# Performance work log

Measured on AMD Instinct MI355X. Metric: run time of the kernel, lower is better.

## Reference

```python
import jax, jax.numpy as jnp
import numpy as np

N_NODES = 50000
N_EDGES = 800000
D = 128


def _graph_conv(x, W, b, src, dst, n_nodes):
    """DGL GraphConv with norm='both': D_in^{-1/2} A D_out^{-1/2} X W + b."""
    ones = jnp.ones((src.shape[0],), dtype=x.dtype)
    out_deg = jax.ops.segment_sum(ones, src, num_segments=n_nodes)
    in_deg = jax.ops.segment_sum(ones, dst, num_segments=n_nodes)
    out_norm = jax.lax.rsqrt(jnp.maximum(out_deg, 1.0))  # [N]
    in_norm = jax.lax.rsqrt(jnp.maximum(in_deg, 1.0))    # [N]
    # scale src features, transform (in_feats == out_feats so order is free), aggregate
    h = (x * out_norm[:, None]) @ W                       # [N, D]
    msgs = h[src]                                         # [E, D] gather
    agg = jax.ops.segment_sum(msgs, dst, num_segments=n_nodes)  # [N, D] scatter-add
    return agg * in_norm[:, None] + b


def setup_inputs() -> dict:
    key = jax.random.key(0)
    ks = jax.random.split(key, 8)
    x = jax.random.normal(ks[0], (N_NODES, D), dtype=jnp.float32)
    src = jax.random.randint(ks[1], (N_EDGES,), 0, N_NODES, dtype=jnp.int64)
    dst = jax.random.randint(ks[2], (N_EDGES,), 0, N_NODES, dtype=jnp.int64)
    scale = 1.0 / np.sqrt(D)
    W1 = jax.random.normal(ks[3], (D, D), dtype=jnp.float32) * scale
    W2 = jax.random.normal(ks[4], (D, D), dtype=jnp.float32) * scale
    W3 = jax.random.normal(ks[5], (D, D), dtype=jnp.float32) * scale
    b1 = jnp.zeros((D,), dtype=jnp.float32)
    b2 = jnp.zeros((D,), dtype=jnp.float32)
    b3 = jnp.zeros((D,), dtype=jnp.float32)
    return {"x": x, "src": src, "dst": dst,
            "W1": W1, "b1": b1, "W2": W2, "b2": b2, "W3": W3, "b3": b3}


def reference(x, src, dst, W1, b1, W2, b2, W3, b3):
    h = _graph_conv(x, W1, b1, src, dst, N_NODES)
    h = jax.nn.relu(h)
    h = _graph_conv(h, W2, b2, src, dst, N_NODES)
    h = jax.nn.relu(h)
    h = _graph_conv(h, W3, b3, src, dst, N_NODES)
    return h
```

## Files before the change

### kernel.cpp

```cpp
#include <hip/hip_runtime.h>
#include <hip/hip_fp16.h>

#define D 128
#define HB 128
#define HT 1024
#define WMAX 12800

struct alignas(16) H8 { __half2 h[4]; };
typedef _Float16 v8h __attribute__((ext_vector_type(8)));
typedef float v4f __attribute__((ext_vector_type(4)));

__global__ __launch_bounds__(HT) void hist_kernel(const int* __restrict__ src,
                                                  const int* __restrict__ dst,
                                                  unsigned* __restrict__ partial_out,
                                                  unsigned* __restrict__ partial_in,
                                                  unsigned char* __restrict__ lrank,
                                                  const float* __restrict__ W1,
                                                  const float* __restrict__ W2,
                                                  const float* __restrict__ W3,
                                                  _Float16* __restrict__ wt,
                                                  int nE, int W, int epb) {
    const int t = threadIdx.x;
    if ((int)blockIdx.x >= 2 * HB) {
        const int l = blockIdx.x - 2 * HB;
        const float* Wsrc = (l == 0) ? W1 : ((l == 1) ? W2 : W3);
        _Float16* o = wt + (size_t)l * D * D;
        for (int i = t; i < D * D; i += HT) {
            const int k = i >> 7, n = i & 127;
            o[n * D + k] = (_Float16)Wsrc[i];
        }
        return;
    }
    __shared__ unsigned lcnt[WMAX];
    const bool is_dst = (blockIdx.x < HB);
    const int b = is_dst ? blockIdx.x : (blockIdx.x - HB);
    for (int i = t; i < W; i += HT) lcnt[i] = 0;
    __syncthreads();
    const int e0 = b * epb;
    const int e1 = min(nE, e0 + epb);
    if (is_dst) {
        for (int e = e0 + t; e < e1; e += HT) {
            const int d = dst[e];
            const unsigned sh = (unsigned)(d & 3) * 8u;
            const unsigned old = atomicAdd(&lcnt[d >> 2], 1u << sh);
            lrank[e] = (unsigned char)((old >> sh) & 0xffu);
        }
    } else {
        for (int e = e0 + t; e < e1; e += HT) {
            const int s = src[e];
            atomicAdd(&lcnt[s >> 2], 1u << ((unsigned)(s & 3) * 8u));
        }
    }
    __syncthreads();
    unsigned* g = (is_dst ? partial_in : partial_out) + (size_t)b * W;
    for (int i = t; i < W; i += HT) g[i] = lcnt[i];
}

__global__ __launch_bounds__(256) void reduce_hist_kernel(const unsigned* __restrict__ partial_out,
                                                          const unsigned* __restrict__ partial_in,
                                                          unsigned* __restrict__ offs_in,
                                                          int* __restrict__ cnt_out,
                                                          int* __restrict__ cnt_in,
                                                          int W, int n, int nbW) {
    const bool is_dst = ((int)blockIdx.x < nbW);
    const int w = (is_dst ? blockIdx.x : (blockIdx.x - nbW)) * 256 + threadIdx.x;
    if (w >= W) return;
    unsigned run = 0;
    if (is_dst) {
#pragma unroll 16
        for (int b = 0; b < HB; ++b) {
            const unsigned c = partial_in[(size_t)b * W + w];
            offs_in[(size_t)b * W + w] = run;
            run += c;
        }
    } else {
#pragma unroll 16
        for (int b = 0; b < HB; ++b) run += partial_out[(size_t)b * W + w];
    }
    int* cnt = is_dst ? cnt_in : cnt_out;
    const int n0 = w * 4;
    const int4 c4 = make_int4((int)(run & 0xffu), (int)((run >> 8) & 0xffu),
                              (int)((run >> 16) & 0xffu), (int)((run >> 24) & 0xffu));
    if (n0 + 3 < n) {
        *(int4*)&cnt[n0] = c4;
    } else {
        const int* cp = &c4.x;
        for (int i = 0; i < 4 && n0 + i < n; ++i) cnt[n0 + i] = cp[i];
    }
}

__global__ __launch_bounds__(1024) void scan_block_kernel(const int* __restrict__ deg,
                                                          int* __restrict__ rp,
                                                          int* __restrict__ bsum, int n) {
    __shared__ int wsum[16];
    const int t = threadIdx.x;
    const int lane = t & 63;
    const int wid = t >> 6;
    const int i = blockIdx.x * 1024 + t;
    const int v = (i < n) ? deg[i] : 0;
    int s = v;
#pragma unroll
    for (int off = 1; off < 64; off <<= 1) {
        int u = __shfl_up(s, off, 64);
        if (lane >= off) s += u;
    }
    if (lane == 63) wsum[wid] = s;
    __syncthreads();
    if (wid == 0) {
        int ws = (lane < 16) ? wsum[lane] : 0;
#pragma unroll
        for (int off = 1; off < 16; off <<= 1) {
            int u = __shfl_up(ws, off, 64);
            if (lane >= off) ws += u;
        }
        if (lane < 16) wsum[lane] = ws;
    }
    __syncthreads();
    const int excl = s - v + ((wid > 0) ? wsum[wid - 1] : 0);
    if (i < n) rp[i] = excl;
    if (t == 0) bsum[blockIdx.x] = wsum[15];
}

__global__ __launch_bounds__(1024) void finalize_kernel(int* __restrict__ rp,
                                                        const int* __restrict__ bsum,
                                                        const int* __restrict__ cnt_out,
                                                        const int* __restrict__ cnt_in,
                                                        float* __restrict__ onorm,
                                                        float* __restrict__ inorm,
                                                        int n, int nb, int nE) {
    __shared__ int prefix_s;
    const int t = threadIdx.x;
    if (t < 64) {
        int v = (t < nb && t < (int)blockIdx.x) ? bsum[t] : 0;
#pragma unroll
        for (int off = 1; off < 64; off <<= 1) v += __shfl_xor(v, off, 64);
        if (t == 0) prefix_s = v;
    }
    __syncthreads();
    const int i = blockIdx.x * 1024 + t;
    if (i < n) {
        rp[i] += prefix_s;
        onorm[i] = rsqrtf(fmaxf((float)cnt_out[i], 1.0f));
        inorm[i] = rsqrtf(fmaxf((float)cnt_in[i], 1.0f));
    }
    if (blockIdx.x == 0 && t == 0) rp[n] = nE;
}

__global__ __launch_bounds__(1024) void gemm1_fill_kernel(
    const float* __restrict__ x, const _Float16* __restrict__ wt,
    const float* __restrict__ onorm, __half* __restrict__ y1, int nrows,
    const int* __restrict__ src, const int* __restrict__ dst,
    const unsigned char* __restrict__ lrank, const unsigned* __restrict__ offs_in,
    const int* __restrict__ rp, int* __restrict__ srcs_sorted,
    int nE, int epb, int W, int nGemmBlocks) {
    __shared__ _Float16 sA[128 * 136];
    __shared__ _Float16 sB[128 * 136];
    const int t = threadIdx.x;

    if ((int)blockIdx.x >= nGemmBlocks) {
        const int e = (blockIdx.x - nGemmBlocks) * 1024 + t;
        if (e < nE) {
            const int d = dst[e];
            const int b = e / epb;
            const unsigned off =
                (offs_in[(size_t)b * W + (d >> 2)] >> ((unsigned)(d & 3) * 8u)) & 0xffu;
            srcs_sorted[rp[d] + (int)off + (int)lrank[e]] = src[e];
        }
        return;
    }

    const int row0 = blockIdx.x * 128;
    const int rr = t >> 4;
    const int c8 = t & 15;
#pragma unroll
    for (int pass = 0; pass < 2; ++pass) {
        const int row = pass * 64 + rr;
        *(float4*)&sB[row * 136 + c8 * 8] = *(const float4*)&wt[(size_t)row * D + c8 * 8];
        const int grow = row0 + row;
        float4 u0 = make_float4(0.f, 0.f, 0.f, 0.f);
        float4 u1 = u0;
        if (grow < nrows) {
            const float* ap = x + (size_t)grow * D + c8 * 8;
            u0 = ((const float4*)ap)[0];
            u1 = ((const float4*)ap)[1];
        }
        v8h hv;
        hv[0] = (_Float16)u0.x; hv[1] = (_Float16)u0.y;
        hv[2] = (_Float16)u0.z; hv[3] = (_Float16)u0.w;
        hv[4] = (_Float16)u1.x; hv[5] = (_Float16)u1.y;
        hv[6] = (_Float16)u1.z; hv[7] = (_Float16)u1.w;
        *(v8h*)&sA[row * 136 + c8 * 8] = hv;
    }
    __syncthreads();

    const int w = t >> 6;
    const int lane = t & 63;
    const int m16 = lane & 15;
    const int quad = lane >> 4;
    const int rt = w >> 1;
    const int ch = w & 1;

    v4f c[4];
#pragma unroll
    for (int ct = 0; ct < 4; ++ct) c[ct] = (v4f){0.f, 0.f, 0.f, 0.f};

#pragma unroll
    for (int ks = 0; ks < 4; ++ks) {
        const v8h a = *(const v8h*)&sA[(rt * 16 + m16) * 136 + ks * 32 + quad * 8];
#pragma unroll
        for (int ct = 0; ct < 4; ++ct) {
            const v8h b = *(const v8h*)&sB[((ch * 4 + ct) * 16 + m16) * 136 + ks * 32 + quad * 8];
            c[ct] = __builtin_amdgcn_mfma_f32_16x16x32_f16(a, b, c[ct], 0, 0, 0);
        }
    }

#pragma unroll
    for (int r = 0; r < 4; ++r) {
        const int row = row0 + rt * 16 + quad * 4 + r;
        if (row < nrows) {
            const float osc = onorm[row];
#pragma unroll
            for (int ct = 0; ct < 4; ++ct) {
                const int col = (ch * 4 + ct) * 16 + m16;
                y1[(size_t)row * D + col] = __float2half(c[ct][r] * osc);
            }
        }
    }
}

template <bool EPI>
__global__ __launch_bounds__(256) void aggregate_kernel(const __half* __restrict__ xh,
                                                        const float* __restrict__ onorm,
                                                        const float* __restrict__ inorm,
                                                        const float* __restrict__ bias,
                                                        const int* __restrict__ rp,
                                                        const int* __restrict__ srcs,
                                                        __half* __restrict__ agg, int n_nodes) {
    const int node = blockIdx.x * 4 + (threadIdx.x >> 6);
    const int lane = threadIdx.x & 63;
    const int rg = lane >> 4;
    const int c8 = lane & 15;
    if (node >= n_nodes) return;
    const int e0 = rp[node];
    const int e1 = rp[node + 1];

    float acc0[8], acc1[8];
#pragma unroll
    for (int j = 0; j < 8; ++j) { acc0[j] = 0.f; acc1[j] = 0.f; }

    auto accum = [&](float* acc, const H8 v) {
#pragma unroll
        for (int j = 0; j < 4; ++j) {
            acc[2 * j]     += __low2float(v.h[j]);
            acc[2 * j + 1] += __high2float(v.h[j]);
        }
    };

    int e = e0;
    for (; e + 16 <= e1; e += 16) {
        const int s0 = srcs[e + rg];
        const int s1 = srcs[e + 4 + rg];
        const int s2 = srcs[e + 8 + rg];
        const int s3 = srcs[e + 12 + rg];
        const H8 v0 = ((const H8*)(xh + (size_t)s0 * D))[c8];
        const H8 v1 = ((const H8*)(xh + (size_t)s1 * D))[c8];
        const H8 v2 = ((const H8*)(xh + (size_t)s2 * D))[c8];
        const H8 v3 = ((const H8*)(xh + (size_t)s3 * D))[c8];
        accum(acc0, v0); accum(acc1, v1); accum(acc0, v2); accum(acc1, v3);
    }
    for (; e + 4 <= e1; e += 4) {
        const int s0 = srcs[e + rg];
        accum(acc0, ((const H8*)(xh + (size_t)s0 * D))[c8]);
    }
    if (e < e1 && rg < (e1 - e)) {
        const int s0 = srcs[e + rg];
        accum(acc1, ((const H8*)(xh + (size_t)s0 * D))[c8]);
    }

    float r[8];
#pragma unroll
    for (int j = 0; j < 8; ++j) r[j] = acc0[j] + acc1[j];
#pragma unroll
    for (int off = 16; off < 64; off <<= 1)
#pragma unroll
        for (int j = 0; j < 8; ++j) r[j] += __shfl_xor(r[j], off, 64);

    if (rg == 0) {
        if (EPI) {
            const float inm = inorm[node];
            const float onm = onorm[node];
            const float4 bv0 = ((const float4*)bias)[c8 * 2];
            const float4 bv1 = ((const float4*)bias)[c8 * 2 + 1];
            const float* bp0 = &bv0.x;
            const float* bp1 = &bv1.x;
#pragma unroll
            for (int j = 0; j < 4; ++j) {
                r[j]     = fmaxf(fmaf(r[j],     inm, bp0[j]), 0.f) * onm;
                r[j + 4] = fmaxf(fmaf(r[j + 4], inm, bp1[j]), 0.f) * onm;
            }
        }
        H8 h;
#pragma unroll
        for (int j = 0; j < 4; ++j) h.h[j] = __floats2half2_rn(r[2 * j], r[2 * j + 1]);
        ((H8*)(agg + (size_t)node * D))[c8] = h;
    }
}

template <bool FULL, bool RELU, bool OSCALE, bool OUT16>
__global__ __launch_bounds__(256) void gemm_mfma_kernel(const __half* __restrict__ Ah,
                                                        const _Float16* __restrict__ Wt,
                                                        const float* __restrict__ bias,
                                                        const float* __restrict__ inorm,
                                                        const float* __restrict__ onorm,
                                                        void* __restrict__ outv, int nrows) {
    __shared__ _Float16 sA[128 * 136];
    __shared__ _Float16 sB[128 * 136];
    const int t = threadIdx.x;
    const int row0 = blockIdx.x * 128;
    const int rr = t >> 4;
    const int c8 = t & 15;

#pragma unroll
    for (int pass = 0; pass < 8; ++pass) {
        const int row = pass * 16 + rr;
        *(float4*)&sB[row * 136 + c8 * 8] = *(const float4*)&Wt[(size_t)row * D + c8 * 8];
        const int grow = row0 + row;
        float4 v = make_float4(0.f, 0.f, 0.f, 0.f);
        if (grow < nrows)
            v = *(const float4*)((const _Float16*)Ah + (size_t)grow * D + c8 * 8);
        *(float4*)&sA[row * 136 + c8 * 8] = v;
    }
    __syncthreads();

    const int w = t >> 6;
    const int lane = t & 63;
    const int m16 = lane & 15;
    const int quad = lane >> 4;

    v4f c[2][8];
#pragma unroll
    for (int rt = 0; rt < 2; ++rt)
#pragma unroll
        for (int ct = 0; ct < 8; ++ct) c[rt][ct] = (v4f){0.f, 0.f, 0.f, 0.f};

#pragma unroll
    for (int ks = 0; ks < 4; ++ks) {
        v8h afr[2], bfr[8];
#pragma unroll
        for (int rt = 0; rt < 2; ++rt)
            afr[rt] = *(const v8h*)&sA[(w * 32 + rt * 16 + m16) * 136 + ks * 32 + quad * 8];
#pragma unroll
        for (int ct = 0; ct < 8; ++ct)
            bfr[ct] = *(const v8h*)&sB[(ct * 16 + m16) * 136 + ks * 32 + quad * 8];
#pragma unroll
        for (int rt = 0; rt < 2; ++rt)
#pragma unroll
            for (int ct = 0; ct < 8; ++ct)
                c[rt][ct] = __builtin_amdgcn_mfma_f32_16x16x32_f16(afr[rt], bfr[ct], c[rt][ct], 0, 0, 0);
    }

#pragma unroll
    for (int rt = 0; rt < 2; ++rt) {
#pragma unroll
        for (int r = 0; r < 4; ++r) {
            const int row = row0 + w * 32 + rt * 16 + quad * 4 + r;
            if (row < nrows) {
                const float inm = FULL ? inorm[row] : 1.0f;
                const float osc = OSCALE ? onorm[row] : 1.0f;
#pragma unroll
                for (int ct = 0; ct < 8; ++ct) {
                    const int col = ct * 16 + m16;
                    float v = c[rt][ct][r];
                    if (FULL) v = fmaf(v, inm, bias[col]);
                    if (RELU) v = fmaxf(v, 0.f);
                    if (OSCALE) v *= osc;
                    if (OUT16) ((__half*)outv)[(size_t)row * D + col] = __float2half(v);
                    else       ((float*)outv)[(size_t)row * D + col] = v;
                }
            }
        }
    }
}

extern "C" void kernel_launch(void* const* d_in, const int* in_sizes, int n_in,
                              void* d_out, int out_size, void* d_ws, size_t ws_size,
                              hipStream_t stream) {
    const float* x   = (const float*)d_in[0];
    const int*   src = (const int*)d_in[1];
    const int*   dst = (const int*)d_in[2];
    const float* W1  = (const float*)d_in[3];
    const float* b1  = (const float*)d_in[4];
    const float* W2  = (const float*)d_in[5];
    const float* b2  = (const float*)d_in[6];
    const float* W3  = (const float*)d_in[7];
    const float* b3  = (const float*)d_in[8];

    const int N = in_sizes[0] / D;
    const int E = in_sizes[1];

    char* p = (char*)d_ws;
    auto alloc = [&](size_t bytes) -> void* {
        void* r = (void*)p;
        p += (bytes + 255) & ~(size_t)255;
        return r;
    };
    int*           cnt_out = (int*)alloc((size_t)N * 4);
    int*           cnt_in  = (int*)alloc((size_t)N * 4);
    int*           rp      = (int*)alloc((size_t)(N + 1) * 4);
    int*           bsum    = (int*)alloc(1024 * 4);
    float*         onorm   = (float*)alloc((size_t)N * 4);
    float*         inorm   = (float*)alloc((size_t)N * 4);
    int*           srcs    = (int*)alloc((size_t)E * 4);
    unsigned char* lrank   = (unsigned char*)alloc((size_t)E);
    _Float16*      wt      = (_Float16*)alloc((size_t)3 * D * D * 2);
    __half*        hbuf0   = (__half*)alloc((size_t)N * D * 2);
    __half*        hbuf1   = (__half*)alloc((size_t)N * D * 2);
    char*          scratch = (char*)alloc((size_t)3 * HB * ((N + 3) / 4) * 4);

    const int W = (N + 3) / 4;
    const int epb = (E + HB - 1) / HB;
    unsigned* partial_in  = (unsigned*)scratch;
    unsigned* partial_out = partial_in + (size_t)HB * W;
    unsigned* offs_in     = partial_out + (size_t)HB * W;
    __half*   abuf        = (__half*)scratch;
    float*    outf        = (float*)d_out;

    const int nb = (N + 1023) / 1024;
    const int nbW = (W + 255) / 256;
    const int gemmGrid = (N + 127) / 128;
    const int fillGrid = (E + 1023) / 1024;
    const int aggGrid = (N + 3) / 4;

    hist_kernel<<<2 * HB + 3, HT, 0, stream>>>(src, dst, partial_out, partial_in, lrank,
                                               W1, W2, W3, wt, E, W, epb);
    reduce_hist_kernel<<<2 * nbW, 256, 0, stream>>>(partial_out, partial_in, offs_in,
                                                    cnt_out, cnt_in, W, N, nbW);
    scan_block_kernel<<<nb, 1024, 0, stream>>>(cnt_in, rp, bsum, N);
    finalize_kernel<<<nb, 1024, 0, stream>>>(rp, bsum, cnt_out, cnt_in, onorm, inorm, N, nb, E);

    gemm1_fill_kernel<<<gemmGrid + fillGrid, 1024, 0, stream>>>(
        x, wt, onorm, hbuf0, N,
        src, dst, lrank, offs_in, rp, srcs, E, epb, W, gemmGrid);

    aggregate_kernel<true><<<aggGrid, 256, 0, stream>>>(
        hbuf0, onorm, inorm, b1, rp, srcs, hbuf1, N);
    aggregate_kernel<false><<<aggGrid, 256, 0, stream>>>(
        hbuf1, onorm, inorm, b2, rp, srcs, abuf, N);
    gemm_mfma_kernel<true, true, true, true><<<gemmGrid, 256, 0, stream>>>(
        abuf, wt + (size_t)D * D, b2, inorm, onorm, hbuf0, N);
    aggregate_kernel<false><<<aggGrid, 256, 0, stream>>>(
        hbuf0, onorm, inorm, b3, rp, srcs, abuf, N);
    gemm_mfma_kernel<true, false, false, false><<<gemmGrid, 256, 0, stream>>>(
        abuf, wt + (size_t)2 * D * D, b3, inorm, onorm, outf, N);
}
```

Measured before the change: 245.1 us.

## Fuse neighbor aggregation into GEMM for layers two and three

```diff
diff --git a/kernel.cpp b/kernel.cpp
--- a/kernel.cpp
+++ b/kernel.cpp
@@ -228,7 +228,6 @@
     }
 }
 
-template <bool EPI>
 __global__ __launch_bounds__(256) void aggregate_kernel(const __half* __restrict__ xh,
                                                         const float* __restrict__ onorm,
                                                         const float* __restrict__ inorm,
@@ -286,18 +285,16 @@
         for (int j = 0; j < 8; ++j) r[j] += __shfl_xor(r[j], off, 64);
 
     if (rg == 0) {
-        if (EPI) {
-            const float inm = inorm[node];
-            const float onm = onorm[node];
-            const float4 bv0 = ((const float4*)bias)[c8 * 2];
-            const float4 bv1 = ((const float4*)bias)[c8 * 2 + 1];
-            const float* bp0 = &bv0.x;
-            const float* bp1 = &bv1.x;
-#pragma unroll
-            for (int j = 0; j < 4; ++j) {
-                r[j]     = fmaxf(fmaf(r[j],     inm, bp0[j]), 0.f) * onm;
-                r[j + 4] = fmaxf(fmaf(r[j + 4], inm, bp1[j]), 0.f) * onm;
-            }
+        const float inm = inorm[node];
+        const float onm = onorm[node];
+        const float4 bv0 = ((const float4*)bias)[c8 * 2];
+        const float4 bv1 = ((const float4*)bias)[c8 * 2 + 1];
+        const float* bp0 = &bv0.x;
+        const float* bp1 = &bv1.x;
+#pragma unroll
+        for (int j = 0; j < 4; ++j) {
+            r[j]     = fmaxf(fmaf(r[j],     inm, bp0[j]), 0.f) * onm;
+            r[j + 4] = fmaxf(fmaf(r[j + 4], inm, bp1[j]), 0.f) * onm;
         }
         H8 h;
 #pragma unroll
@@ -306,76 +303,121 @@
     }
 }
 
-template <bool FULL, bool RELU, bool OSCALE, bool OUT16>
-__global__ __launch_bounds__(256) void gemm_mfma_kernel(const __half* __restrict__ Ah,
-                                                        const _Float16* __restrict__ Wt,
-                                                        const float* __restrict__ bias,
-                                                        const float* __restrict__ inorm,
-                                                        const float* __restrict__ onorm,
-                                                        void* __restrict__ outv, int nrows) {
-    __shared__ _Float16 sA[128 * 136];
+template <bool LAST>
+__global__ __launch_bounds__(256) void agg_gemm_kernel(const __half* __restrict__ xh,
+                                                       const _Float16* __restrict__ Wt,
+                                                       const float* __restrict__ bias,
+                                                       const float* __restrict__ inorm,
+                                                       const float* __restrict__ onorm,
+                                                       const int* __restrict__ rp,
+                                                       const int* __restrict__ srcs,
+                                                       void* __restrict__ outv, int n_nodes) {
+    __shared__ _Float16 sA[64 * 136];
     __shared__ _Float16 sB[128 * 136];
     const int t = threadIdx.x;
-    const int row0 = blockIdx.x * 128;
-    const int rr = t >> 4;
-    const int c8 = t & 15;
-
-#pragma unroll
-    for (int pass = 0; pass < 8; ++pass) {
-        const int row = pass * 16 + rr;
-        *(float4*)&sB[row * 136 + c8 * 8] = *(const float4*)&Wt[(size_t)row * D + c8 * 8];
-        const int grow = row0 + row;
-        float4 v = make_float4(0.f, 0.f, 0.f, 0.f);
-        if (grow < nrows)
-            v = *(const float4*)((const _Float16*)Ah + (size_t)grow * D + c8 * 8);
-        *(float4*)&sA[row * 136 + c8 * 8] = v;
-    }
-    __syncthreads();
+    const int tile0 = blockIdx.x * 64;
+
+    {
+        const int rr = t >> 4;
+        const int cc = t & 15;
+#pragma unroll
+        for (int p = 0; p < 8; ++p) {
+            const int row = p * 16 + rr;
+            *(float4*)&sB[row * 136 + cc * 8] = *(const float4*)&Wt[(size_t)row * D + cc * 8];
+        }
+    }
 
     const int w = t >> 6;
     const int lane = t & 63;
+    const int rg = lane >> 4;
+    const int c8 = lane & 15;
+
+    for (int i = 0; i < 16; ++i) {
+        const int lrow = w * 16 + i;
+        const int node = tile0 + lrow;
+        float r[8];
+#pragma unroll
+        for (int j = 0; j < 8; ++j) r[j] = 0.f;
+        if (node < n_nodes) {
+            const int e0 = rp[node];
+            const int e1 = rp[node + 1];
+            float acc1[8];
+#pragma unroll
+            for (int j = 0; j < 8; ++j) acc1[j] = 0.f;
+            auto accum = [&](float* acc, const H8 v) {
+#pragma unroll
+                for (int j = 0; j < 4; ++j) {
+                    acc[2 * j]     += __low2float(v.h[j]);
+                    acc[2 * j + 1] += __high2float(v.h[j]);
+                }
+            };
+            int e = e0;
+            for (; e + 16 <= e1; e += 16) {
+                const int s0 = srcs[e + rg];
+                const int s1 = srcs[e + 4 + rg];
+                const int s2 = srcs[e + 8 + rg];
+                const int s3 = srcs[e + 12 + rg];
+                const H8 v0 = ((const H8*)(xh + (size_t)s0 * D))[c8];
+                const H8 v1 = ((const H8*)(xh + (size_t)s1 * D))[c8];
+                const H8 v2 = ((const H8*)(xh + (size_t)s2 * D))[c8];
+                const H8 v3 = ((const H8*)(xh + (size_t)s3 * D))[c8];
+                accum(r, v0); accum(acc1, v1); accum(r, v2); accum(acc1, v3);
+            }
+            for (; e + 4 <= e1; e += 4) {
+                const int s0 = srcs[e + rg];
+                accum(r, ((const H8*)(xh + (size_t)s0 * D))[c8]);
+            }
+            if (e < e1 && rg < (e1 - e)) {
+                const int s0 = srcs[e + rg];
+                accum(acc1, ((const H8*)(xh + (size_t)s0 * D))[c8]);
+            }
+#pragma unroll
+            for (int j = 0; j < 8; ++j) r[j] += acc1[j];
+#pragma unroll
+            for (int off = 16; off < 64; off <<= 1)
+#pragma unroll
+                for (int j = 0; j < 8; ++j) r[j] += __shfl_xor(r[j], off, 64);
+        }
+        if (rg == 0) {
+            H8 h;
+#pragma unroll
+            for (int j = 0; j < 4; ++j) h.h[j] = __floats2half2_rn(r[2 * j], r[2 * j + 1]);
+            *(H8*)&sA[lrow * 136 + c8 * 8] = h;
+        }
+    }
+    __syncthreads();
+
     const int m16 = lane & 15;
     const int quad = lane >> 4;
-
-    v4f c[2][8];
-#pragma unroll
-    for (int rt = 0; rt < 2; ++rt)
-#pragma unroll
-        for (int ct = 0; ct < 8; ++ct) c[rt][ct] = (v4f){0.f, 0.f, 0.f, 0.f};
+    v4f c[8];
+#pragma unroll
+    for (int ct = 0; ct < 8; ++ct) c[ct] = (v4f){0.f, 0.f, 0.f, 0.f};
 
 #pragma unroll
     for (int ks = 0; ks < 4; ++ks) {
-        v8h afr[2], bfr[8];
-#pragma unroll
-        for (int rt = 0; rt < 2; ++rt)
-            afr[rt] = *(const v8h*)&sA[(w * 32 + rt * 16 + m16) * 136 + ks * 32 + quad * 8];
-#pragma unroll
-        for (int ct = 0; ct < 8; ++ct)
-            bfr[ct] = *(const v8h*)&sB[(ct * 16 + m16) * 136 + ks * 32 + quad * 8];
-#pragma unroll
-        for (int rt = 0; rt < 2; ++rt)
-#pragma unroll
-            for (int ct = 0; ct < 8; ++ct)
-                c[rt][ct] = __builtin_amdgcn_mfma_f32_16x16x32_f16(afr[rt], bfr[ct], c[rt][ct], 0, 0, 0);
-    }
-
-#pragma unroll
-    for (int rt = 0; rt < 2; ++rt) {
-#pragma unroll
-        for (int r = 0; r < 4; ++r) {
-            const int row = row0 + w * 32 + rt * 16 + quad * 4 + r;
-            if (row < nrows) {
-                const float inm = FULL ? inorm[row] : 1.0f;
-                const float osc = OSCALE ? onorm[row] : 1.0f;
-#pragma unroll
-                for (int ct = 0; ct < 8; ++ct) {
-                    const int col = ct * 16 + m16;
-                    float v = c[rt][ct][r];
-                    if (FULL) v = fmaf(v, inm, bias[col]);
-                    if (RELU) v = fmaxf(v, 0.f);
-                    if (OSCALE) v *= osc;
-                    if (OUT16) ((__half*)outv)[(size_t)row * D + col] = __float2half(v);
-                    else       ((float*)outv)[(size_t)row * D + col] = v;
+        const v8h a = *(const v8h*)&sA[(w * 16 + m16) * 136 + ks * 32 + quad * 8];
+#pragma unroll
+        for (int ct = 0; ct < 8; ++ct) {
+            const v8h b = *(const v8h*)&sB[(ct * 16 + m16) * 136 + ks * 32 + quad * 8];
+            c[ct] = __builtin_amdgcn_mfma_f32_16x16x32_f16(a, b, c[ct], 0, 0, 0);
+        }
+    }
+
+#pragma unroll
+    for (int r = 0; r < 4; ++r) {
+        const int row = tile0 + w * 16 + quad * 4 + r;
+        if (row < n_nodes) {
+            const float inm = inorm[row];
+            const float osc = LAST ? 1.0f : onorm[row];
+#pragma unroll
+            for (int ct = 0; ct < 8; ++ct) {
+                const int col = ct * 16 + m16;
+                float v = fmaf(c[ct][r], inm, bias[col]);
+                if (!LAST) {
+                    v = fmaxf(v, 0.f) * osc;
+                    ((__half*)outv)[(size_t)row * D + col] = __float2half(v);
+                } else {
+                    ((float*)outv)[(size_t)row * D + col] = v;
                 }
             }
         }
@@ -422,7 +464,6 @@
     unsigned* partial_in  = (unsigned*)scratch;
     unsigned* partial_out = partial_in + (size_t)HB * W;
     unsigned* offs_in     = partial_out + (size_t)HB * W;
-    __half*   abuf        = (__half*)scratch;
     float*    outf        = (float*)d_out;
 
     const int nb = (N + 1023) / 1024;
@@ -430,6 +471,7 @@
     const int gemmGrid = (N + 127) / 128;
     const int fillGrid = (E + 1023) / 1024;
     const int aggGrid = (N + 3) / 4;
+    const int fuseGrid = (N + 63) / 64;
 
     hist_kernel<<<2 * HB + 3, HT, 0, stream>>>(src, dst, partial_out, partial_in, lrank,
                                                W1, W2, W3, wt, E, W, epb);
@@ -442,14 +484,10 @@
         x, wt, onorm, hbuf0, N,
         src, dst, lrank, offs_in, rp, srcs, E, epb, W, gemmGrid);
 
-    aggregate_kernel<true><<<aggGrid, 256, 0, stream>>>(
+    aggregate_kernel<<<aggGrid, 256, 0, stream>>>(
         hbuf0, onorm, inorm, b1, rp, srcs, hbuf1, N);
-    aggregate_kernel<false><<<aggGrid, 256, 0, stream>>>(
-        hbuf1, onorm, inorm, b2, rp, srcs, abuf, N);
-    gemm_mfma_kernel<true, true, true, true><<<gemmGrid, 256, 0, stream>>>(
-        abuf, wt + (size_t)D * D, b2, inorm, onorm, hbuf0, N);
-    aggregate_kernel<false><<<aggGrid, 256, 0, stream>>>(
-        hbuf0, onorm, inorm, b3, rp, srcs, abuf, N);
-    gemm_mfma_kernel<true, false, false, false><<<gemmGrid, 256, 0, stream>>>(
-        abuf, wt + (size_t)2 * D * D, b3, inorm, onorm, outf, N);
-}
+    agg_gemm_kernel<false><<<fuseGrid, 256, 0, stream>>>(
+        hbuf1, wt + (size_t)D * D, b2, inorm, onorm, rp, srcs, hbuf0, N);
+    agg_gemm_kernel<true><<<fuseGrid, 256, 0, stream>>>(
+        hbuf0, wt + (size_t)2 * D * D, b3, inorm, onorm, rp, srcs, outf, N);
+}
```

Result: slower. 325.6 us (+32.8%).
